# Performance work log

Hardware: AMD Instinct MI355X
Metric: run time of the kernel (lower is better)

The kernel has to match this reference:

```python
import jax, jax.numpy as jnp
import numpy as np

B, N, PS = 8, 2048, 32
P = N // PS          # 64 patches
D, MLP, DEPTH, H, DH = 1024, 2048, 6, 8, 64
INNER = H * DH       # 512
K = 20
EPS = 1e-5


def setup_inputs() -> dict:
    key = jax.random.key(0)
    ks = jax.random.split(key, 16)
    r = lambda i, shape: jax.random.normal(ks[i], shape, dtype=jnp.float32) * 0.02
    return {
        "x": jax.random.normal(ks[0], (B, N, 3), dtype=jnp.float32),
        "x_pos_embed": r(1, (B, P + 1, D)),
        "w1": r(2, (64, 6)),   "g1": jnp.ones(64),  "b1": jnp.zeros(64),
        "w2": r(3, (64, 128)), "g2": jnp.ones(64),  "b2": jnp.zeros(64),
        "w3": r(4, (128, 128)),"g3": jnp.ones(128), "b3": jnp.zeros(128),
        "w4": r(5, (256, 256)),"g4": jnp.ones(256), "b4": jnp.zeros(256),
        "w5": r(6, (D, 512)),  "g5": jnp.ones(D),   "b5": jnp.zeros(D),
        "cls_token": r(7, (1, 1, D)),
        "ln1_g": jnp.ones((DEPTH, D)), "ln1_b": jnp.zeros((DEPTH, D)),
        "wqkv": r(8, (DEPTH, D, 3 * INNER)),
        "wout": r(9, (DEPTH, INNER, D)), "bout": jnp.zeros((DEPTH, D)),
        "ln2_g": jnp.ones((DEPTH, D)), "ln2_b": jnp.zeros((DEPTH, D)),
        "wff1": r(10, (DEPTH, D, MLP)), "bff1": jnp.zeros((DEPTH, MLP)),
        "wff2": r(11, (DEPTH, MLP, D)), "bff2": jnp.zeros((DEPTH, D)),
    }


def _knn(x, k):  # x: [B, C, N] -> neighbor idx [B, N, k]
    xx = jnp.sum(x * x, axis=1)                        # [B, N]
    inner = jnp.einsum('bcn,bcm->bnm', x, x)           # [B, N, N]
    dist = 2.0 * inner - xx[:, :, None] - xx[:, None, :]  # = -||xi-xj||^2
    return jax.lax.top_k(dist, k)[1]


def _graph_feature(x, k):  # x: [B, C, N] -> [B, N, k, 2C]
    idx = _knn(x, k)
    xt = jnp.transpose(x, (0, 2, 1))                   # [B, N, C]
    nbr = jax.vmap(lambda f, i: f[i])(xt, idx)         # gather: [B, N, k, C]
    ctr = jnp.broadcast_to(xt[:, :, None, :], nbr.shape)
    return jnp.concatenate([nbr - ctr, ctr], axis=-1)


def _leaky(v):
    return jnp.where(v >= 0, v, 0.2 * v)


def _edge_conv(x, w, g, b, k):  # EdgeConv block: graph feat -> 1x1 conv -> BN(train) -> lrelu -> max over k
    f = _graph_feature(x, k)                           # [B, N, k, 2C]
    y = jnp.einsum('bnkc,oc->bonk', f, w)              # [B, O, N, k]
    mu = jnp.mean(y, axis=(0, 2, 3), keepdims=True)
    var = jnp.var(y, axis=(0, 2, 3), keepdims=True)
    y = (y - mu) * jax.lax.rsqrt(var + EPS) * g[None, :, None, None] + b[None, :, None, None]
    return jnp.max(_leaky(y), axis=-1)                 # [B, O, N]


def _ln(x, g, b):
    mu = jnp.mean(x, axis=-1, keepdims=True)
    var = jnp.var(x, axis=-1, keepdims=True)
    return (x - mu) * jax.lax.rsqrt(var + EPS) * g + b


def reference(x, x_pos_embed, w1, g1, b1, w2, g2, b2, w3, g3, b3, w4, g4, b4,
              w5, g5, b5, cls_token, ln1_g, ln1_b, wqkv, wout, bout,
              ln2_g, ln2_b, wff1, bff1, wff2, bff2):
    scale = DH ** -0.5
    pts = jnp.transpose(x, (0, 2, 1))                  # [B, 3, N]
    x1 = _edge_conv(pts, w1, g1, b1, K)                # [B, 64, N]
    x2 = _edge_conv(x1, w2, g2, b2, K)                 # [B, 64, N]
    x3 = _edge_conv(x2, w3, g3, b3, K)                 # [B, 128, N]
    x4 = _edge_conv(x3, w4, g4, b4, K)                 # [B, 256, N]
    h = jnp.concatenate([x1, x2, x3, x4], axis=1)      # [B, 512, N]
    y = jnp.einsum('bcn,oc->bon', h, w5)               # conv5 1x1 -> [B, D, N]
    mu = jnp.mean(y, axis=(0, 2), keepdims=True)
    var = jnp.var(y, axis=(0, 2), keepdims=True)
    y = _leaky((y - mu) * jax.lax.rsqrt(var + EPS) * g5[None, :, None] + b5[None, :, None])
    # patch max-pool: 'b (p n) c -> (b p) n c' then max over n
    t = jnp.transpose(y, (0, 2, 1)).reshape(B * P, PS, D)
    t = jnp.max(t, axis=1).reshape(B, P, D)
    t = jnp.concatenate([jnp.broadcast_to(cls_token, (B, 1, D)), t], axis=1)  # [B, P+1, D]
    for i in range(DEPTH):
        t = t + x_pos_embed
        hn = _ln(t, ln1_g[i], ln1_b[i])
        qkv = (hn @ wqkv[i]).reshape(B, P + 1, 3, H, DH)
        q, k_, v = [jnp.transpose(qkv[:, :, j], (0, 2, 1, 3)) for j in range(3)]
        attn = jax.nn.softmax(jnp.einsum('bhld,bhmd->bhlm', q, k_) * scale, axis=-1)
        z = jnp.einsum('bhlm,bhmd->bhld', attn, v)
        z = jnp.transpose(z, (0, 2, 1, 3)).reshape(B, P + 1, INNER)
        t = t + z @ wout[i] + bout[i]
        hn = _ln(t, ln2_g[i], ln2_b[i])
        t = t + jax.nn.gelu(hn @ wff1[i] + bff1[i], approximate=False) @ wff2[i] + bff2[i]
    return t[:, 1:]                                    # [B, P, D]
```

## Files before the change

### kernel.cpp

```cpp
#include <hip/hip_runtime.h>
#include <math.h>

#define BB 8
#define NN 2048
#define PSZ 32
#define PP 64
#define DD 1024
#define MLPD 2048
#define DEPTH_ 6
#define HH 8
#define DHH 64
#define INNER_ 512
#define KK 20
#define TOK 65
#define EPSF 1e-5f

#define GEMM_ACC 1
#define GEMM_GELU 2
#define GEMM_OUTBF16 4

typedef __bf16 bf16_t;
typedef __attribute__((ext_vector_type(8))) __bf16 bf16x8;
typedef __attribute__((ext_vector_type(4))) float f32x4;

__global__ void transpose_x_kernel(const float* __restrict__ x, float* __restrict__ pts) {
    int gid = blockIdx.x * blockDim.x + threadIdx.x;
    if (gid >= BB * NN * 3) return;
    int c = gid % 3; int n = (gid / 3) % NN; int b = gid / (3 * NN);
    pts[(b * 3 + c) * NN + n] = x[gid];
}

__global__ void sqnorm_kernel(const float* __restrict__ x, int bs, int C, float* __restrict__ xx) {
    int gid = blockIdx.x * blockDim.x + threadIdx.x;
    if (gid >= BB * NN) return;
    int n = gid % NN; int b = gid / NN;
    const float* xp = x + b * bs + n;
    float s = 0.f;
    for (int c = 0; c < C; ++c) { float v = xp[c * NN]; s += v * v; }
    xx[gid] = s;
}

__global__ __launch_bounds__(256) void dist_kernel(const float* __restrict__ x, int bs, int C,
                                                   const float* __restrict__ xx, int b0,
                                                   float* __restrict__ dist) {
    __shared__ __align__(16) float As[16][132];
    __shared__ __align__(16) float Bs[16][132];
    int b = b0 + blockIdx.z;
    int n0 = blockIdx.y * 128, m0 = blockIdx.x * 128;
    int tid = threadIdx.x;
    int ty = tid >> 4, tx = tid & 15;
    float acc[2][2][4][4] = {};
    const float* xb = x + (long)b * bs;
    for (int k0 = 0; k0 < C; k0 += 16) {
        #pragma unroll
        for (int p = 0; p < 2; ++p) {
            int li = tid + p * 256;
            int i4 = li & 31;
            int kk = li >> 5;
            int c = k0 + kk;
            float4 va = make_float4(0.f, 0.f, 0.f, 0.f);
            float4 vb = va;
            if (c < C) {
                va = *(const float4*)&xb[(long)c * NN + n0 + i4 * 4];
                vb = *(const float4*)&xb[(long)c * NN + m0 + i4 * 4];
            }
            *(float4*)&As[kk][i4 * 4] = va;
            *(float4*)&Bs[kk][i4 * 4] = vb;
        }
        __syncthreads();
        #pragma unroll
        for (int kk = 0; kk < 16; ++kk) {
            float a[2][4], bv[2][4];
            *(float4*)a[0] = *(const float4*)&As[kk][ty * 4];
            *(float4*)a[1] = *(const float4*)&As[kk][64 + ty * 4];
            *(float4*)bv[0] = *(const float4*)&Bs[kk][tx * 4];
            *(float4*)bv[1] = *(const float4*)&Bs[kk][64 + tx * 4];
            #pragma unroll
            for (int ri = 0; ri < 2; ++ri)
                #pragma unroll
                for (int ci = 0; ci < 2; ++ci)
                    #pragma unroll
                    for (int i = 0; i < 4; ++i)
                        #pragma unroll
                        for (int j = 0; j < 4; ++j)
                            acc[ri][ci][i][j] += a[ri][i] * bv[ci][j];
        }
        __syncthreads();
    }
    float* db = dist + (long)blockIdx.z * NN * NN;
    const float* xxb = xx + b * NN;
    float xm[2][4];
    #pragma unroll
    for (int ci = 0; ci < 2; ++ci)
        #pragma unroll
        for (int j = 0; j < 4; ++j)
            xm[ci][j] = xxb[m0 + ci * 64 + tx * 4 + j];
    #pragma unroll
    for (int ri = 0; ri < 2; ++ri)
        #pragma unroll
        for (int i = 0; i < 4; ++i) {
            int n = n0 + ri * 64 + ty * 4 + i;
            float xn = xxb[n];
            #pragma unroll
            for (int ci = 0; ci < 2; ++ci) {
                int m = m0 + ci * 64 + tx * 4;
                float4 st;
                st.x = 2.f * acc[ri][ci][i][0] - xn - xm[ci][0];
                st.y = 2.f * acc[ri][ci][i][1] - xn - xm[ci][1];
                st.z = 2.f * acc[ri][ci][i][2] - xn - xm[ci][2];
                st.w = 2.f * acc[ri][ci][i][3] - xn - xm[ci][3];
                *(float4*)&db[(long)n * NN + m] = st;
            }
        }
}

__global__ __launch_bounds__(256) void topk_kernel(const float* __restrict__ dist, int b0,
                                                   int* __restrict__ idx) {
    int b = b0 + blockIdx.y;
    int wid = threadIdx.x >> 6, lane = threadIdx.x & 63;
    int n = blockIdx.x * 4 + wid;
    const float* row = dist + ((long)blockIdx.y * NN + n) * NN;
    float vals[32];
    #pragma unroll
    for (int s = 0; s < 32; ++s) vals[s] = row[s * 64 + lane];
    int* op = idx + ((long)b * NN + n) * KK;
    for (int kk = 0; kk < KK; ++kk) {
        float bv = vals[0]; int bsl = 0;
        #pragma unroll
        for (int s = 1; s < 32; ++s) if (vals[s] > bv) { bv = vals[s]; bsl = s; }
        int bm = bsl * 64 + lane;
        for (int off = 32; off; off >>= 1) {
            float ov = __shfl_xor(bv, off);
            int om = __shfl_xor(bm, off);
            if (ov > bv || (ov == bv && om < bm)) { bv = ov; bm = om; }
        }
        int wslot = bm >> 6, wlane = bm & 63;
        #pragma unroll
        for (int s = 0; s < 32; ++s)
            if (s == wslot) vals[s] = (lane == wlane) ? -INFINITY : vals[s];
        if (lane == 0) op[kk] = bm;
    }
}

__global__ __launch_bounds__(256) void pq_kernel(const float* __restrict__ x, int bs, int C,
                                                 const float* __restrict__ w, int O,
                                                 float* __restrict__ p, float* __restrict__ q) {
    __shared__ float wT[256][33];
    __shared__ float xs[128][32];
    int b = blockIdx.z;
    int o0 = blockIdx.y * 32;
    int n0 = blockIdx.x * 32;
    int tid = threadIdx.x;
    for (int i = tid; i < 2 * C * 32; i += 256) {
        int c2 = i % (2 * C), o = i / (2 * C);
        wT[c2][o] = w[(o0 + o) * 2 * C + c2];
    }
    for (int i = tid; i < C * 32; i += 256) {
        int nl = i % 32, c = i / 32;
        xs[c][nl] = x[b * bs + c * NN + n0 + nl];
    }
    __syncthreads();
    int o_l = tid & 31;
    int n_base = (tid >> 5) * 4;
    float ps[4] = {0.f, 0.f, 0.f, 0.f};
    float qs[4] = {0.f, 0.f, 0.f, 0.f};
    for (int c = 0; c < C; ++c) {
        float4 xv = *(const float4*)&xs[c][n_base];
        float wa = wT[c][o_l];
        float wb = wT[C + c][o_l];
        float d = wb - wa;
        ps[0] += xv.x * wa; qs[0] += xv.x * d;
        ps[1] += xv.y * wa; qs[1] += xv.y * d;
        ps[2] += xv.z * wa; qs[2] += xv.z * d;
        ps[3] += xv.w * wa; qs[3] += xv.w * d;
    }
    for (int j = 0; j < 4; ++j) {
        long r = (long)(b * NN + n0 + n_base + j) * O + o0 + o_l;
        p[r] = ps[j];
        q[r] = qs[j];
    }
}

__global__ void zero_stats_kernel(double* __restrict__ s1, double* __restrict__ s2) {
    int t = blockIdx.x * blockDim.x + threadIdx.x;
    if (t < 1024) { s1[t] = 0.0; s2[t] = 0.0; }
}

__global__ __launch_bounds__(256) void edge_stats_kernel(const float* __restrict__ p, const float* __restrict__ q,
                                                         const int* __restrict__ idx, int O,
                                                         double* __restrict__ gsum, double* __restrict__ gsumsq) {
    int tid = threadIdx.x;
    int o = tid % O;
    int grp = tid / O;
    int ngrp = 256 / O;
    int rows_per_blk = (BB * NN) / gridDim.x;
    int r0 = blockIdx.x * rows_per_blk;
    double s = 0.0, ss = 0.0;
    for (int r = r0 + grp; r < r0 + rows_per_blk; r += ngrp) {
        int b = r / NN;
        float qv = q[r * O + o];
        for (int k = 0; k < KK; ++k) {
            int j = idx[r * KK + k];
            float v = p[(b * NN + j) * O + o] + qv;
            s += v; ss += (double)v * v;
        }
    }
    atomicAdd(&gsum[o], s);
    atomicAdd(&gsumsq[o], ss);
}

__global__ void bn_finalize_kernel(const double* __restrict__ gsum, const double* __restrict__ gsumsq,
                                   const float* __restrict__ g, const float* __restrict__ bb, int O, double cnt,
                                   float* __restrict__ scale, float* __restrict__ shift) {
    int o = blockIdx.x * blockDim.x + threadIdx.x;
    if (o >= O) return;
    double mean = gsum[o] / cnt;
    double var = gsumsq[o] / cnt - mean * mean;
    float inv = rsqrtf((float)var + EPSF);
    float sc = g[o] * inv;
    scale[o] = sc;
    shift[o] = bb[o] - (float)mean * sc;
}

__global__ void edge_out_kernel(const float* __restrict__ p, const float* __restrict__ q,
                                const int* __restrict__ idx, int O,
                                const float* __restrict__ scale, const float* __restrict__ shift,
                                float* __restrict__ out, int obs) {
    int gid = blockIdx.x * blockDim.x + threadIdx.x;
    if (gid >= BB * NN * O) return;
    int o = gid % O; int n = (gid / O) % NN; int b = gid / (O * NN);
    int r = b * NN + n;
    float qv = q[r * O + o];
    float sc = scale[o], sh = shift[o];
    float m = -INFINITY;
    for (int k = 0; k < KK; ++k) {
        int j = idx[r * KK + k];
        float v = (p[(b * NN + j) * O + o] + qv) * sc + sh;
        v = (v >= 0.f) ? v : 0.2f * v;
        m = fmaxf(m, v);
    }
    out[b * obs + o * NN + n] = m;
}

__global__ __launch_bounds__(256) void transpose_cvt_kernel(const float* __restrict__ in,
                                                            bf16_t* __restrict__ outp,
                                                            int R, int C, long s_in, long s_out) {
    __shared__ float tile[32][33];
    const float* ib = in + (long)blockIdx.z * s_in;
    bf16_t* ob = outp + (long)blockIdx.z * s_out;
    int r0 = blockIdx.y * 32, c0 = blockIdx.x * 32;
    int tx = threadIdx.x & 31, tg = threadIdx.x >> 5;
    for (int i = 0; i < 4; ++i) {
        int r = tg + i * 8;
        tile[r][tx] = ib[(long)(r0 + r) * C + c0 + tx];
    }
    __syncthreads();
    for (int i = 0; i < 4; ++i) {
        int c = tg + i * 8;
        ob[(long)(c0 + c) * R + r0 + tx] = (bf16_t)tile[tx][c];
    }
}

__global__ __launch_bounds__(256) void gemm_bf16_kernel(const float* __restrict__ A,
                                                        const bf16_t* __restrict__ Bt,
                                                        const float* __restrict__ bias,
                                                        float* __restrict__ out,
                                                        int M, int Kd, int Nd,
                                                        long sA, long sBt, long sO, int flags) {
    __shared__ __align__(16) bf16_t As[64 * 32];
    __shared__ __align__(16) bf16_t Bs[64 * 32];
    const float* Ab = A + (long)blockIdx.z * sA;
    const bf16_t* Bb = Bt + (long)blockIdx.z * sBt;
    int row0 = blockIdx.y * 64, col0 = blockIdx.x * 64;
    int tid = threadIdx.x;
    int lane = tid & 63, wv = tid >> 6;
    int wm = wv >> 1, wn = wv & 1;
    int srow = tid >> 2;
    int skp = (tid & 3) * 8;
    f32x4 acc[2][2] = {};
    for (int k0 = 0; k0 < Kd; k0 += 32) {
        {
            int r = row0 + srow;
            float av[8];
            if (r < M) {
                const float* ap = Ab + (long)r * Kd + k0 + skp;
                float4 a0 = *(const float4*)ap;
                float4 a1 = *(const float4*)(ap + 4);
                av[0] = a0.x; av[1] = a0.y; av[2] = a0.z; av[3] = a0.w;
                av[4] = a1.x; av[5] = a1.y; av[6] = a1.z; av[7] = a1.w;
            } else {
                #pragma unroll
                for (int j = 0; j < 8; ++j) av[j] = 0.f;
            }
            bf16x8 v;
            #pragma unroll
            for (int j = 0; j < 8; ++j) v[j] = (bf16_t)av[j];
            *(bf16x8*)&As[((skp >> 3) * 64 + srow) * 8] = v;
        }
        {
            const bf16_t* bp = Bb + (long)(col0 + srow) * Kd + k0 + skp;
            bf16x8 v = *(const bf16x8*)bp;
            *(bf16x8*)&Bs[((skp >> 3) * 64 + srow) * 8] = v;
        }
        __syncthreads();
        int q = lane >> 4, cl = lane & 15;
        bf16x8 a0v = *(const bf16x8*)&As[(q * 64 + wm * 32 + cl) * 8];
        bf16x8 a1v = *(const bf16x8*)&As[(q * 64 + wm * 32 + 16 + cl) * 8];
        bf16x8 b0v = *(const bf16x8*)&Bs[(q * 64 + wn * 32 + cl) * 8];
        bf16x8 b1v = *(const bf16x8*)&Bs[(q * 64 + wn * 32 + 16 + cl) * 8];
        acc[0][0] = __builtin_amdgcn_mfma_f32_16x16x32_bf16(a0v, b0v, acc[0][0], 0, 0, 0);
        acc[0][1] = __builtin_amdgcn_mfma_f32_16x16x32_bf16(a0v, b1v, acc[0][1], 0, 0, 0);
        acc[1][0] = __builtin_amdgcn_mfma_f32_16x16x32_bf16(a1v, b0v, acc[1][0], 0, 0, 0);
        acc[1][1] = __builtin_amdgcn_mfma_f32_16x16x32_bf16(a1v, b1v, acc[1][1], 0, 0, 0);
        __syncthreads();
    }
    int q = lane >> 4, cl = lane & 15;
    float* Obf = out + (long)blockIdx.z * sO;
    bf16_t* Obh = (bf16_t*)out + (long)blockIdx.z * sO;
    for (int mt = 0; mt < 2; ++mt)
        for (int nt = 0; nt < 2; ++nt)
            #pragma unroll
            for (int r = 0; r < 4; ++r) {
                int row = row0 + wm * 32 + mt * 16 + q * 4 + r;
                if (row >= M) continue;
                int col = col0 + wn * 32 + nt * 16 + cl;
                float v = acc[mt][nt][r];
                if (bias) v += bias[col];
                if (flags & GEMM_GELU) v = 0.5f * v * (1.f + erff(v * 0.70710678118654752f));
                long oidx = (long)row * Nd + col;
                if (flags & GEMM_OUTBF16) Obh[oidx] = (bf16_t)v;
                else if (flags & GEMM_ACC) Obf[oidx] += v;
                else Obf[oidx] = v;
            }
}

__global__ __launch_bounds__(256) void gemm_kernel(const float* __restrict__ A, const float* __restrict__ Bm,
                                                   const float* __restrict__ bias, float* __restrict__ out,
                                                   int M, int Kd, int Nd, long sA, long sB, long sO, int flags) {
    __shared__ float As[16][65];
    __shared__ float Bs[16][64];
    const float* Ab = A + (long)blockIdx.z * sA;
    const float* Bb = Bm + (long)blockIdx.z * sB;
    float* Ob = out + (long)blockIdx.z * sO;
    int row0 = blockIdx.y * 64, col0 = blockIdx.x * 64;
    int tid = threadIdx.x;
    int ty = tid / 16, tx = tid % 16;
    float acc[4][4] = {};
    for (int k0 = 0; k0 < Kd; k0 += 16) {
        for (int i = 0; i < 4; ++i) {
            int li = tid + i * 256;
            int m = li / 16, kk = li % 16;
            int r = row0 + m;
            As[kk][m] = (r < M) ? Ab[(long)r * Kd + k0 + kk] : 0.f;
        }
        for (int i = 0; i < 4; ++i) {
            int li = tid + i * 256;
            int kk = li / 64, n = li % 64;
            int c = col0 + n;
            Bs[kk][n] = (c < Nd) ? Bb[(long)(k0 + kk) * Nd + c] : 0.f;
        }
        __syncthreads();
        for (int kk = 0; kk < 16; ++kk) {
            float a[4], bv[4];
            for (int i = 0; i < 4; ++i) a[i] = As[kk][ty * 4 + i];
            for (int j = 0; j < 4; ++j) bv[j] = Bs[kk][tx * 4 + j];
            for (int i = 0; i < 4; ++i)
                for (int j = 0; j < 4; ++j)
                    acc[i][j] += a[i] * bv[j];
        }
        __syncthreads();
    }
    for (int i = 0; i < 4; ++i) {
        int r = row0 + ty * 4 + i;
        if (r >= M) continue;
        for (int j = 0; j < 4; ++j) {
            int c = col0 + tx * 4 + j;
            if (c >= Nd) continue;
            float v = acc[i][j];
            if (bias) v += bias[c];
            if (flags & GEMM_GELU) v = 0.5f * v * (1.f + erff(v * 0.70710678118654752f));
            long oidx = (long)r * Nd + c;
            if (flags & GEMM_ACC) Ob[oidx] += v; else Ob[oidx] = v;
        }
    }
}

__global__ __launch_bounds__(256) void bn5_stats_bf16_kernel(const bf16_t* __restrict__ y5,
                                                             const float* __restrict__ g,
                                                             const float* __restrict__ bb,
                                                             float* __restrict__ scale, float* __restrict__ shift) {
    __shared__ double ssum[256], ssq[256];
    int d = blockIdx.x;
    int tid = threadIdx.x;
    double s = 0.0, sq = 0.0;
    for (int b = 0; b < BB; ++b) {
        const bf16_t* row = y5 + ((long)b * DD + d) * NN;
        for (int n = tid; n < NN; n += 256) { float v = (float)row[n]; s += v; sq += (double)v * v; }
    }
    ssum[tid] = s; ssq[tid] = sq;
    __syncthreads();
    for (int st = 128; st > 0; st >>= 1) {
        if (tid < st) { ssum[tid] += ssum[tid + st]; ssq[tid] += ssq[tid + st]; }
        __syncthreads();
    }
    if (tid == 0) {
        double cnt = (double)BB * NN;
        double mean = ssum[0] / cnt;
        double var = ssq[0] / cnt - mean * mean;
        float inv = rsqrtf((float)var + EPSF);
        float sc = g[d] * inv;
        scale[d] = sc;
        shift[d] = bb[d] - (float)mean * sc;
    }
}

__global__ __launch_bounds__(256) void bn5_stats_kernel(const float* __restrict__ y5, const float* __restrict__ g,
                                                        const float* __restrict__ bb,
                                                        float* __restrict__ scale, float* __restrict__ shift) {
    __shared__ double ssum[256], ssq[256];
    int d = blockIdx.x;
    int tid = threadIdx.x;
    double s = 0.0, sq = 0.0;
    for (int b = 0; b < BB; ++b) {
        const float* row = y5 + ((long)b * DD + d) * NN;
        for (int n = tid; n < NN; n += 256) { float v = row[n]; s += v; sq += (double)v * v; }
    }
    ssum[tid] = s; ssq[tid] = sq;
    __syncthreads();
    for (int st = 128; st > 0; st >>= 1) {
        if (tid < st) { ssum[tid] += ssum[tid + st]; ssq[tid] += ssq[tid + st]; }
        __syncthreads();
    }
    if (tid == 0) {
        double cnt = (double)BB * NN;
        double mean = ssum[0] / cnt;
        double var = ssq[0] / cnt - mean * mean;
        float inv = rsqrtf((float)var + EPSF);
        float sc = g[d] * inv;
        scale[d] = sc;
        shift[d] = bb[d] - (float)mean * sc;
    }
}

__global__ void pool_bf16_kernel(const bf16_t* __restrict__ y5, const float* __restrict__ scale,
                                 const float* __restrict__ shift, const float* __restrict__ cls,
                                 float* __restrict__ t) {
    int gid = blockIdx.x * blockDim.x + threadIdx.x;
    if (gid >= BB * TOK * DD) return;
    int d = gid % DD; int l = (gid / DD) % TOK; int b = gid / (DD * TOK);
    float v;
    if (l == 0) {
        v = cls[d];
    } else {
        int pp = l - 1;
        const bf16_t* row = y5 + ((long)b * DD + d) * NN + pp * PSZ;
        float sc = scale[d], sh = shift[d];
        float m = -INFINITY;
        for (int i = 0; i < PSZ; ++i) {
            float u = (float)row[i] * sc + sh;
            u = (u >= 0.f) ? u : 0.2f * u;
            m = fmaxf(m, u);
        }
        v = m;
    }
    t[gid] = v;
}

__global__ void pool_kernel(const float* __restrict__ y5, const float* __restrict__ scale,
                            const float* __restrict__ shift, const float* __restrict__ cls,
                            float* __restrict__ t) {
    int gid = blockIdx.x * blockDim.x + threadIdx.x;
    if (gid >= BB * TOK * DD) return;
    int d = gid % DD; int l = (gid / DD) % TOK; int b = gid / (DD * TOK);
    float v;
    if (l == 0) {
        v = cls[d];
    } else {
        int pp = l - 1;
        const float* row = y5 + ((long)b * DD + d) * NN + pp * PSZ;
        float sc = scale[d], sh = shift[d];
        float m = -INFINITY;
        for (int i = 0; i < PSZ; ++i) {
            float u = row[i] * sc + sh;
            u = (u >= 0.f) ? u : 0.2f * u;
            m = fmaxf(m, u);
        }
        v = m;
    }
    t[gid] = v;
}

__global__ __launch_bounds__(256) void ln_kernel(float* __restrict__ t, const float* __restrict__ pos,
                                                 const float* __restrict__ g, const float* __restrict__ bb,
                                                 float* __restrict__ hn, int addpos) {
    __shared__ double s1[256], s2[256];
    long r = blockIdx.x;
    int tid = threadIdx.x;
    float vals[4];
    double s = 0.0, sq = 0.0;
    for (int i = 0; i < 4; ++i) {
        int d = tid + i * 256;
        float v = t[r * DD + d];
        if (addpos) { v += pos[r * DD + d]; t[r * DD + d] = v; }
        vals[i] = v; s += v; sq += (double)v * v;
    }
    s1[tid] = s; s2[tid] = sq;
    __syncthreads();
    for (int st = 128; st > 0; st >>= 1) {
        if (tid < st) { s1[tid] += s1[tid + st]; s2[tid] += s2[tid + st]; }
        __syncthreads();
    }
    double mean = s1[0] / DD;
    float var = (float)(s2[0] / DD - mean * mean);
    float fm = (float)mean;
    float inv = rsqrtf(var + EPSF);
    for (int i = 0; i < 4; ++i) {
        int d = tid + i * 256;
        hn[r * DD + d] = (vals[i] - fm) * inv * g[d] + bb[d];
    }
}

__global__ __launch_bounds__(256) void attn_kernel(const float* __restrict__ qkv, float* __restrict__ z) {
    __shared__ float ks[TOK][DHH + 1];
    __shared__ float vs[TOK][DHH + 1];
    __shared__ float ss[TOK][TOK];
    int bh = blockIdx.x;
    int b = bh / HH, h = bh % HH;
    int tid = threadIdx.x;
    for (int i = tid; i < TOK * DHH; i += 256) {
        int l = i / DHH, d = i % DHH;
        long base = (long)(b * TOK + l) * 1536;
        ks[l][d] = qkv[base + 512 + h * DHH + d];
        vs[l][d] = qkv[base + 1024 + h * DHH + d];
    }
    __syncthreads();
    for (int i = tid; i < TOK * TOK; i += 256) {
        int l = i / TOK, m = i % TOK;
        const float* qrow = qkv + (long)(b * TOK + l) * 1536 + h * DHH;
        float acc = 0.f;
        for (int d = 0; d < DHH; ++d) acc += qrow[d] * ks[m][d];
        ss[l][m] = acc * 0.125f;
    }
    __syncthreads();
    if (tid < TOK) {
        float mx = -INFINITY;
        for (int m = 0; m < TOK; ++m) mx = fmaxf(mx, ss[tid][m]);
        float sum = 0.f;
        for (int m = 0; m < TOK; ++m) { float e = expf(ss[tid][m] - mx); ss[tid][m] = e; sum += e; }
        float invs = 1.f / sum;
        for (int m = 0; m < TOK; ++m) ss[tid][m] *= invs;
    }
    __syncthreads();
    for (int i = tid; i < TOK * DHH; i += 256) {
        int l = i / DHH, d = i % DHH;
        float acc = 0.f;
        for (int m = 0; m < TOK; ++m) acc += ss[l][m] * vs[m][d];
        z[(long)(b * TOK + l) * INNER_ + h * DHH + d] = acc;
    }
}

__global__ void final_kernel(const float* __restrict__ t, float* __restrict__ out) {
    int gid = blockIdx.x * blockDim.x + threadIdx.x;
    if (gid >= BB * PP * DD) return;
    int d = gid % DD; int p = (gid / DD) % PP; int b = gid / (DD * PP);
    out[gid] = t[((long)b * TOK + 1 + p) * DD + d];
}

static inline int ceil_div(long a, long b) { return (int)((a + b - 1) / b); }

extern "C" void kernel_launch(void* const* d_in, const int* in_sizes, int n_in,
                              void* d_out, int out_size, void* d_ws, size_t ws_size,
                              hipStream_t stream) {
    const float* x    = (const float*)d_in[0];
    const float* pos  = (const float*)d_in[1];
    const float* w1   = (const float*)d_in[2];
    const float* g1   = (const float*)d_in[3];
    const float* b1   = (const float*)d_in[4];
    const float* w2   = (const float*)d_in[5];
    const float* g2   = (const float*)d_in[6];
    const float* b2   = (const float*)d_in[7];
    const float* w3   = (const float*)d_in[8];
    const float* g3   = (const float*)d_in[9];
    const float* b3   = (const float*)d_in[10];
    const float* w4   = (const float*)d_in[11];
    const float* g4   = (const float*)d_in[12];
    const float* b4   = (const float*)d_in[13];
    const float* w5   = (const float*)d_in[14];
    const float* g5   = (const float*)d_in[15];
    const float* b5   = (const float*)d_in[16];
    const float* cls  = (const float*)d_in[17];
    const float* ln1g = (const float*)d_in[18];
    const float* ln1b = (const float*)d_in[19];
    const float* wqkv = (const float*)d_in[20];
    const float* wout = (const float*)d_in[21];
    const float* bout = (const float*)d_in[22];
    const float* ln2g = (const float*)d_in[23];
    const float* ln2b = (const float*)d_in[24];
    const float* wff1 = (const float*)d_in[25];
    const float* bff1 = (const float*)d_in[26];
    const float* wff2 = (const float*)d_in[27];
    const float* bff2 = (const float*)d_in[28];
    float* out = (float*)d_out;

    char* ws = (char*)d_ws;
    size_t off = 0;
    auto alloc = [&](size_t bytes) -> char* {
        char* ptr = ws + off;
        off = (off + bytes + 255) & ~(size_t)255;
        return ptr;
    };
    float*  h      = (float*)alloc((size_t)BB * 512 * NN * 4);
    float*  t      = (float*)alloc((size_t)BB * TOK * DD * 4);
    float*  hn     = (float*)alloc((size_t)BB * TOK * DD * 4);
    float*  qkvb   = (float*)alloc((size_t)BB * TOK * 1536 * 4);
    float*  zb     = (float*)alloc((size_t)BB * TOK * INNER_ * 4);
    float*  ub     = (float*)alloc((size_t)BB * TOK * MLPD * 4);
    double* dsum   = (double*)alloc(1024 * 8);
    double* dsq    = (double*)alloc(1024 * 8);
    float*  scaleb = (float*)alloc(1024 * 4);
    float*  shiftb = (float*)alloc(1024 * 4);
    size_t ubase = off;

    size_t uoff = ubase;
    auto ualloc = [&](size_t bytes) -> char* {
        char* ptr = ws + uoff;
        uoff = (uoff + bytes + 255) & ~(size_t)255;
        return ptr;
    };
    float* pts  = (float*)ualloc((size_t)BB * 3 * NN * 4);
    float* xx   = (float*)ualloc((size_t)BB * NN * 4);
    int*   idxb = (int*)  ualloc((size_t)BB * NN * KK * 4);
    float* pbuf = (float*)ualloc((size_t)BB * NN * 256 * 4);
    float* qbuf = (float*)ualloc((size_t)BB * NN * 256 * 4);
    size_t dist_rel = uoff - ubase;
    float* distb = (float*)(ws + uoff);

    size_t voff = ubase;
    auto valloc = [&](size_t bytes) -> char* {
        char* ptr = ws + voff;
        voff = (voff + bytes + 255) & ~(size_t)255;
        return ptr;
    };
    bf16_t* hT     = (bf16_t*)valloc((size_t)BB * NN * 512 * 2);
    bf16_t* wTqkv  = (bf16_t*)valloc((size_t)DEPTH_ * 1536 * DD * 2);
    bf16_t* wTout  = (bf16_t*)valloc((size_t)DEPTH_ * DD * INNER_ * 2);
    bf16_t* wTff1  = (bf16_t*)valloc((size_t)DEPTH_ * MLPD * DD * 2);
    bf16_t* wTff2  = (bf16_t*)valloc((size_t)DEPTH_ * DD * MLPD * 2);
    size_t stage_bf16 = voff - ubase;

    size_t conv_full  = dist_rel + (size_t)BB * NN * NN * 4;
    size_t conv_batch = dist_rel + (size_t)NN * NN * 4;
    size_t stage_fp32 = (size_t)BB * DD * NN * 4;

    auto mx = [](size_t a, size_t b) { return a > b ? a : b; };
    bool use_bf16 = ws_size >= ubase + mx(conv_batch, stage_bf16);
    bool full     = ws_size >= ubase + mx(conv_full, use_bf16 ? stage_bf16 : stage_fp32);
    if (!use_bf16 && ws_size < ubase + mx(conv_batch, stage_fp32)) return;
    bf16_t* y5bf = (bf16_t*)h;
    float*  y5f  = (float*)(ws + ubase);

    transpose_x_kernel<<<ceil_div((long)BB * NN * 3, 256), 256, 0, stream>>>(x, pts);

    auto run_conv = [&](const float* xin, int xbs, int C, const float* w,
                        const float* g, const float* bb, float* hout, int O) {
        sqnorm_kernel<<<ceil_div((long)BB * NN, 256), 256, 0, stream>>>(xin, xbs, C, xx);
        if (full) {
            dist_kernel<<<dim3(NN / 128, NN / 128, BB), 256, 0, stream>>>(xin, xbs, C, xx, 0, distb);
            topk_kernel<<<dim3(NN / 4, BB), 256, 0, stream>>>(distb, 0, idxb);
        } else {
            for (int b = 0; b < BB; ++b) {
                dist_kernel<<<dim3(NN / 128, NN / 128, 1), 256, 0, stream>>>(xin, xbs, C, xx, b, distb);
                topk_kernel<<<dim3(NN / 4, 1), 256, 0, stream>>>(distb, b, idxb);
            }
        }
        {
            dim3 grid(NN / 32, O / 32, BB);
            pq_kernel<<<grid, 256, 0, stream>>>(xin, xbs, C, w, O, pbuf, qbuf);
        }
        zero_stats_kernel<<<4, 256, 0, stream>>>(dsum, dsq);
        edge_stats_kernel<<<256, 256, 0, stream>>>(pbuf, qbuf, idxb, O, dsum, dsq);
        bn_finalize_kernel<<<1, 256, 0, stream>>>(dsum, dsq, g, bb, O, (double)BB * NN * KK, scaleb, shiftb);
        edge_out_kernel<<<ceil_div((long)BB * NN * O, 256), 256, 0, stream>>>(
            pbuf, qbuf, idxb, O, scaleb, shiftb, hout, 512 * NN);
    };
    run_conv(pts, 3 * NN, 3, w1, g1, b1, h, 64);
    run_conv(h, 512 * NN, 64, w2, g2, b2, h + 64 * NN, 64);
    run_conv(h + 64 * NN, 512 * NN, 64, w3, g3, b3, h + 128 * NN, 128);
    run_conv(h + 128 * NN, 512 * NN, 128, w4, g4, b4, h + 256 * NN, 256);

    const int M = BB * TOK;
    if (use_bf16) {
        transpose_cvt_kernel<<<dim3(NN / 32, 512 / 32, BB), 256, 0, stream>>>(
            h, hT, 512, NN, (long)512 * NN, (long)NN * 512);
        transpose_cvt_kernel<<<dim3(1536 / 32, DD / 32, DEPTH_), 256, 0, stream>>>(
            wqkv, wTqkv, DD, 1536, (long)DD * 1536, (long)1536 * DD);
        transpose_cvt_kernel<<<dim3(DD / 32, INNER_ / 32, DEPTH_), 256, 0, stream>>>(
            wout, wTout, INNER_, DD, (long)INNER_ * DD, (long)DD * INNER_);
        transpose_cvt_kernel<<<dim3(MLPD / 32, DD / 32, DEPTH_), 256, 0, stream>>>(
            wff1, wTff1, DD, MLPD, (long)DD * MLPD, (long)MLPD * DD);
        transpose_cvt_kernel<<<dim3(DD / 32, MLPD / 32, DEPTH_), 256, 0, stream>>>(
            wff2, wTff2, MLPD, DD, (long)MLPD * DD, (long)DD * MLPD);

        gemm_bf16_kernel<<<dim3(NN / 64, DD / 64, BB), 256, 0, stream>>>(
            w5, hT, nullptr, (float*)y5bf, DD, 512, NN, 0L, (long)NN * 512, (long)DD * NN, GEMM_OUTBF16);
        bn5_stats_bf16_kernel<<<DD, 256, 0, stream>>>(y5bf, g5, b5, scaleb, shiftb);
        pool_bf16_kernel<<<ceil_div((long)BB * TOK * DD, 256), 256, 0, stream>>>(y5bf, scaleb, shiftb, cls, t);

        for (int i = 0; i < DEPTH_; ++i) {
            ln_kernel<<<M, 256, 0, stream>>>(t, pos, ln1g + i * DD, ln1b + i * DD, hn, 1);
            gemm_bf16_kernel<<<dim3(1536 / 64, ceil_div(M, 64), 1), 256, 0, stream>>>(
                hn, wTqkv + (size_t)i * 1536 * DD, nullptr, qkvb, M, DD, 1536, 0L, 0L, 0L, 0);
            attn_kernel<<<BB * HH, 256, 0, stream>>>(qkvb, zb);
            gemm_bf16_kernel<<<dim3(DD / 64, ceil_div(M, 64), 1), 256, 0, stream>>>(
                zb, wTout + (size_t)i * DD * INNER_, bout + i * DD, t, M, INNER_, DD, 0L, 0L, 0L, GEMM_ACC);
            ln_kernel<<<M, 256, 0, stream>>>(t, nullptr, ln2g + i * DD, ln2b + i * DD, hn, 0);
            gemm_bf16_kernel<<<dim3(MLPD / 64, ceil_div(M, 64), 1), 256, 0, stream>>>(
                hn, wTff1 + (size_t)i * MLPD * DD, bff1 + i * MLPD, ub, M, DD, MLPD, 0L, 0L, 0L, GEMM_GELU);
            gemm_bf16_kernel<<<dim3(DD / 64, ceil_div(M, 64), 1), 256, 0, stream>>>(
                ub, wTff2 + (size_t)i * DD * MLPD, bff2 + i * DD, t, M, MLPD, DD, 0L, 0L, 0L, GEMM_ACC);
        }
    } else {
        gemm_kernel<<<dim3(NN / 64, DD / 64, BB), 256, 0, stream>>>(
            w5, h, nullptr, y5f, DD, 512, NN, 0L, (long)512 * NN, (long)DD * NN, 0);
        bn5_stats_kernel<<<DD, 256, 0, stream>>>(y5f, g5, b5, scaleb, shiftb);
        pool_kernel<<<ceil_div((long)BB * TOK * DD, 256), 256, 0, stream>>>(y5f, scaleb, shiftb, cls, t);
        for (int i = 0; i < DEPTH_; ++i) {
            ln_kernel<<<M, 256, 0, stream>>>(t, pos, ln1g + i * DD, ln1b + i * DD, hn, 1);
            gemm_kernel<<<dim3(1536 / 64, ceil_div(M, 64), 1), 256, 0, stream>>>(
                hn, wqkv + (size_t)i * DD * 1536, nullptr, qkvb, M, DD, 1536, 0L, 0L, 0L, 0);
            attn_kernel<<<BB * HH, 256, 0, stream>>>(qkvb, zb);
            gemm_kernel<<<dim3(DD / 64, ceil_div(M, 64), 1), 256, 0, stream>>>(
                zb, wout + (size_t)i * INNER_ * DD, bout + i * DD, t, M, INNER_, DD, 0L, 0L, 0L, GEMM_ACC);
            ln_kernel<<<M, 256, 0, stream>>>(t, nullptr, ln2g + i * DD, ln2b + i * DD, hn, 0);
            gemm_kernel<<<dim3(DD / 64, ceil_div(M, 64), 1), 256, 0, stream>>>(
                ub, wff2 + (size_t)i * MLPD * DD, bff2 + i * DD, t, M, MLPD, DD, 0L, 0L, 0L, GEMM_ACC);
        }
    }

    final_kernel<<<ceil_div((long)BB * PP * DD, 256), 256, 0, stream>>>(t, out);
}
```

Measured before the change: 2.354 ms.

## Replace iterative top-k selection with threshold bitonic sort and compaction

The per-row top-20 search no longer does 20 rounds of full argmax over 2048 values with wave reductions. Each lane now takes its local max, a bitonic sort of those 64 maxima gives the 20th-largest as a threshold, and values at or above it are compacted into shared memory with ballot and mbcnt. A second bitonic sort on at most 64 candidates then picks the top 20, falling back to the old loop if too many candidates pass. The diff also restores the missing FF1 GELU GEMM in the non-bf16 transformer path, which fixes a correctness hole in that branch.

```diff
diff --git a/kernel.cpp b/kernel.cpp
--- a/kernel.cpp
+++ b/kernel.cpp
@@ -116,6 +116,8 @@
 
 __global__ __launch_bounds__(256) void topk_kernel(const float* __restrict__ dist, int b0,
                                                    int* __restrict__ idx) {
+    __shared__ float cval[4][64];
+    __shared__ int   cidx[4][64];
     int b = b0 + blockIdx.y;
     int wid = threadIdx.x >> 6, lane = threadIdx.x & 63;
     int n = blockIdx.x * 4 + wid;
@@ -124,21 +126,72 @@
     #pragma unroll
     for (int s = 0; s < 32; ++s) vals[s] = row[s * 64 + lane];
     int* op = idx + ((long)b * NN + n) * KK;
-    for (int kk = 0; kk < KK; ++kk) {
-        float bv = vals[0]; int bsl = 0;
+
+    float lm = vals[0];
+    #pragma unroll
+    for (int s = 1; s < 32; ++s) lm = fmaxf(lm, vals[s]);
+
+    float sv = lm;
+    #pragma unroll
+    for (int k = 2; k <= 64; k <<= 1) {
         #pragma unroll
-        for (int s = 1; s < 32; ++s) if (vals[s] > bv) { bv = vals[s]; bsl = s; }
-        int bm = bsl * 64 + lane;
-        for (int off = 32; off; off >>= 1) {
-            float ov = __shfl_xor(bv, off);
-            int om = __shfl_xor(bm, off);
-            if (ov > bv || (ov == bv && om < bm)) { bv = ov; bm = om; }
-        }
-        int wslot = bm >> 6, wlane = bm & 63;
+        for (int j = k >> 1; j > 0; j >>= 1) {
+            float pv = __shfl_xor(sv, j);
+            bool lower = (lane & j) == 0;
+            bool up = (lane & k) != 0;
+            bool ownBetter = sv > pv;
+            bool keepOwn = ownBetter ^ (lower == up);
+            sv = keepOwn ? sv : pv;
+        }
+    }
+    float t = __shfl(sv, 19);
+
+    int base = 0;
+    #pragma unroll
+    for (int s = 0; s < 32; ++s) {
+        bool q = vals[s] >= t;
+        unsigned long long m = __ballot(q);
+        int my = base + (int)__builtin_amdgcn_mbcnt_hi((unsigned)(m >> 32),
+                         __builtin_amdgcn_mbcnt_lo((unsigned)m, 0u));
+        if (q && my < 64) { cval[wid][my] = vals[s]; cidx[wid][my] = s * 64 + lane; }
+        base += (int)__popcll(m);
+    }
+    __asm__ volatile("s_waitcnt lgkmcnt(0)" ::: "memory");
+
+    if (base <= 64) {
+        float v = (lane < base) ? cval[wid][lane] : -INFINITY;
+        int   ii = (lane < base) ? cidx[wid][lane] : 0x7FFFFFFF;
         #pragma unroll
-        for (int s = 0; s < 32; ++s)
-            if (s == wslot) vals[s] = (lane == wlane) ? -INFINITY : vals[s];
-        if (lane == 0) op[kk] = bm;
+        for (int k = 2; k <= 64; k <<= 1) {
+            #pragma unroll
+            for (int j = k >> 1; j > 0; j >>= 1) {
+                float pv = __shfl_xor(v, j);
+                int   pi = __shfl_xor(ii, j);
+                bool lower = (lane & j) == 0;
+                bool up = (lane & k) != 0;
+                bool ownBetter = (v > pv) || (v == pv && ii < pi);
+                bool keepOwn = ownBetter ^ (lower == up);
+                if (!keepOwn) { v = pv; ii = pi; }
+            }
+        }
+        if (lane < KK) op[lane] = ii;
+    } else {
+        for (int kk = 0; kk < KK; ++kk) {
+            float bv = vals[0]; int bsl = 0;
+            #pragma unroll
+            for (int s = 1; s < 32; ++s) if (vals[s] > bv) { bv = vals[s]; bsl = s; }
+            int bm = bsl * 64 + lane;
+            for (int off = 32; off; off >>= 1) {
+                float ov = __shfl_xor(bv, off);
+                int om = __shfl_xor(bm, off);
+                if (ov > bv || (ov == bv && om < bm)) { bv = ov; bm = om; }
+            }
+            int wslot = bm >> 6, wlane = bm & 63;
+            #pragma unroll
+            for (int s = 0; s < 32; ++s)
+                if (s == wslot) vals[s] = (lane == wlane) ? -INFINITY : vals[s];
+            if (lane == 0) op[kk] = bm;
+        }
     }
 }
 
@@ -732,6 +785,8 @@
             gemm_kernel<<<dim3(DD / 64, ceil_div(M, 64), 1), 256, 0, stream>>>(
                 zb, wout + (size_t)i * INNER_ * DD, bout + i * DD, t, M, INNER_, DD, 0L, 0L, 0L, GEMM_ACC);
             ln_kernel<<<M, 256, 0, stream>>>(t, nullptr, ln2g + i * DD, ln2b + i * DD, hn, 0);
+            gemm_kernel<<<dim3(MLPD / 64, ceil_div(M, 64), 1), 256, 0, stream>>>(
+                hn, wff1 + (size_t)i * DD * MLPD, bff1 + i * MLPD, ub, M, DD, MLPD, 0L, 0L, 0L, GEMM_GELU);
             gemm_kernel<<<dim3(DD / 64, ceil_div(M, 64), 1), 256, 0, stream>>>(
                 ub, wff2 + (size_t)i * MLPD * DD, bff2 + i * DD, t, M, MLPD, DD, 0L, 0L, 0L, GEMM_ACC);
         }
```

Result: faster. 2.039 ms (-13.3%).
